# Optimization experiments

Hardware: AMD Instinct MI355X
Metric: run time of the kernel (lower is better)

## Reference

```python
import jax, jax.numpy as jnp
import numpy as np

N_QUBITS = 14
N_LAYERS = 2
LATENT_DIM = 14
DIM = 2 ** N_QUBITS
PAIRS = [(i, i + 1) for i in range(N_QUBITS - 1)]  # 'linear' entanglement


def _cnot_perm(control, target, n):
    # permutation of basis indices implementing CNOT(control, target)
    idx = np.arange(2 ** n)
    cbit = (idx >> (n - control - 1)) & 1
    flipped = np.where(cbit == 1, idx ^ (1 << (n - target - 1)), idx)
    return jnp.asarray(flipped)

CNOT_PERMS = [_cnot_perm(c, t, N_QUBITS) for c, t in PAIRS]


def _apply_1q(state, gate, q):
    # state: (B, 2^n) complex; gate: (2,2) or (B,2,2) complex
    B = state.shape[0]
    s = state.reshape(B, 2 ** (N_QUBITS - q - 1), 2, 2 ** q)
    if gate.ndim == 2:
        s = jnp.einsum('ij,bkjl->bkil', gate, s)
    else:
        s = jnp.einsum('bij,bkjl->bkil', gate, s)
    return s.reshape(B, DIM)


def _ry_batched(theta):
    c = jnp.cos(theta / 2)
    s = jnp.sin(theta / 2)
    g = jnp.stack([jnp.stack([c, -s], -1), jnp.stack([s, c], -1)], -2)  # (B,2,2)
    return g.astype(jnp.complex64)


def _ry(theta):
    c = jnp.cos(theta / 2)
    s = jnp.sin(theta / 2)
    return jnp.stack([jnp.stack([c, -s]), jnp.stack([s, c])]).astype(jnp.complex64)


def _rz(theta):
    th = theta.astype(jnp.complex64)
    e0 = jnp.exp(-0.5j * th)
    e1 = jnp.exp(0.5j * th)
    zero = jnp.zeros((), jnp.complex64)
    return jnp.stack([jnp.stack([e0, zero]), jnp.stack([zero, e1])])


def setup_inputs() -> dict:
    key = jax.random.key(0)
    k1, k2 = jax.random.split(key)
    latent = jax.random.normal(k1, (256, LATENT_DIM), dtype=jnp.float32)
    weights = jax.random.normal(k2, (N_LAYERS * N_QUBITS * 3,), dtype=jnp.float32) * 0.1
    return {"latent": latent, "weights": weights}


def reference(latent, weights):
    B = latent.shape[0]
    state = jnp.zeros((B, DIM), dtype=jnp.complex64).at[:, 0].set(1.0)
    # latent encoding: RY(pi * z_i) on qubit i
    for i in range(min(LATENT_DIM, N_QUBITS)):
        state = _apply_1q(state, _ry_batched(latent[:, i] * np.pi), i)
    # variational layers
    for layer in range(N_LAYERS):
        off = layer * N_QUBITS * 3
        for q in range(N_QUBITS):
            b = off + q * 3
            state = _apply_1q(state, _ry(weights[b]), q)
            state = _apply_1q(state, _rz(weights[b + 1]), q)
            state = _apply_1q(state, _ry(weights[b + 2]), q)
        for perm in CNOT_PERMS:
            state = state[:, perm]
    return jnp.abs(state) ** 2
```

## Files before the change

kernel.cpp:

```cpp
#include <hip/hip_runtime.h>


typedef float f32x2 __attribute__((ext_vector_type(2)));
typedef float f32x4 __attribute__((ext_vector_type(4)));

constexpr int NQ    = 14;
constexpr int DIM   = 1 << NQ;
constexpr int NT    = 512;
constexpr int SPLIT = 2;

__device__ __forceinline__ f32x2 cmul(f32x2 a, f32x2 b) {
    return f32x2{a.x * b.x - a.y * b.y, a.x * b.y + a.y * b.x};
}
__device__ __forceinline__ int g7(int x)  { return x ^ (x >> 1); }
__device__ __forceinline__ int g7i(int x) { x ^= x >> 1; x ^= x >> 2; x ^= x >> 4; return x; }

__global__ __launch_bounds__(NT)
void qsim_kernel(const float* __restrict__ latent,
                 const float* __restrict__ weights,
                 float* __restrict__ out)
{
    __shared__ f32x2 vq [2 * NQ];
    __shared__ f32x2 m1 [4 * NQ];
    __shared__ f32x2 plo[128], phi[128];
    __shared__ f32x2 cc0[128], cc1[128], dd0[128], dd1[128];
    __shared__ __align__(16) float fjx[128], fjy[128], fjz[128], fjw[128];
    __shared__ f32x4 eA[128];

    const int b   = blockIdx.x >> 1;
    const int qtr = blockIdx.x & 1;
    const int tid = threadIdx.x;

    if (tid < NQ) {
        const int q = tid;
        const float a = weights[3 * q] + 3.14159265358979323846f * latent[b * NQ + q];
        const float t = weights[3 * q + 1];
        const float c = weights[3 * q + 2];
        float ct, stt, cp, sp, cm, sm;
        __sincosf(0.5f * t, &stt, &ct);
        __sincosf(0.5f * (a + c), &sp, &cp);
        __sincosf(0.5f * (a - c), &sm, &cm);
        vq[2 * q + 0] = f32x2{ct * cp, -stt * cm};
        vq[2 * q + 1] = f32x2{ct * sp,  stt * sm};
    } else if (tid >= 64 && tid < 64 + NQ) {
        const int q = tid - 64;
        const float a = weights[3 * NQ + 3 * q];
        const float t = weights[3 * NQ + 3 * q + 1];
        const float c = weights[3 * NQ + 3 * q + 2];
        float ct, stt, cp, sp, cm, sm;
        __sincosf(0.5f * t, &stt, &ct);
        __sincosf(0.5f * (a + c), &sp, &cp);
        __sincosf(0.5f * (a - c), &sm, &cm);
        m1[4 * q + 0] = f32x2{ ct * cp, -stt * cm};
        m1[4 * q + 1] = f32x2{-ct * sp,  stt * sm};
        m1[4 * q + 2] = f32x2{ ct * sp,  stt * sm};
        m1[4 * q + 3] = f32x2{ ct * cp,  stt * cm};
    }
    __syncthreads();

    if (tid < 256) {
        const int half = tid >> 7;
        const int m    = tid & 127;
        const int qb   = half * 7;
        f32x2 p = {1.0f, 0.0f};
        #pragma unroll
        for (int j = 0; j < 7; ++j)
            p = cmul(p, vq[2 * (qb + j) + ((m >> j) & 1)]);
        (half ? phi : plo)[m] = p;
    }
    __syncthreads();

    if (tid < 256) {
        const int w    = tid >> 6;
        const int lane = tid & 63;
        const int u0 = 2 * lane, u1 = 2 * lane + 1;

        f32x2 r0, r1;
        if (w == 0)      { r0 = plo[g7(u0)];       r1 = plo[g7(u1)];       }
        else if (w == 1) { r0 = plo[g7(u0) ^ 64];  r1 = plo[g7(u1) ^ 64];  }
        else if (w == 2) { r0 = phi[g7(u0)];       r1 = f32x2{0.f, 0.f};   }
        else             { r0 = f32x2{0.f, 0.f};   r1 = phi[g7(u1)];       }

        const int mbase = (w >> 1) * 7;

        {
            const f32x2 M00 = m1[4 * mbase + 0], M01 = m1[4 * mbase + 1];
            const f32x2 M10 = m1[4 * mbase + 2], M11 = m1[4 * mbase + 3];
            const f32x2 n0 = cmul(M00, r0) + cmul(M01, r1);
            const f32x2 n1 = cmul(M10, r0) + cmul(M11, r1);
            r0 = n0; r1 = n1;
        }
        #pragma unroll
        for (int k = 1; k < 7; ++k) {
            const int q = mbase + k;
            const f32x2 M00 = m1[4 * q + 0], M01 = m1[4 * q + 1];
            const f32x2 M10 = m1[4 * q + 2], M11 = m1[4 * q + 3];
            const int msk = 1 << (k - 1);
            const int bit = (lane >> (k - 1)) & 1;
            f32x2 p0, p1;
            p0.x = __shfl_xor(r0.x, msk, 64); p0.y = __shfl_xor(r0.y, msk, 64);
            p1.x = __shfl_xor(r1.x, msk, 64); p1.y = __shfl_xor(r1.y, msk, 64);
            const f32x2 lo0 = bit ? p0 : r0, hi0 = bit ? r0 : p0;
            const f32x2 lo1 = bit ? p1 : r1, hi1 = bit ? r1 : p1;
            const f32x2 Ma  = bit ? M10 : M00;
            const f32x2 Mb  = bit ? M11 : M01;
            r0 = cmul(Ma, lo0) + cmul(Mb, hi0);
            r1 = cmul(Ma, lo1) + cmul(Mb, hi1);
        }
        const int j0 = g7i(u0), j1 = g7i(u1);
        if (w == 0)      { cc0[j0] = r0; cc0[j1] = r1; }
        else if (w == 1) { cc1[j0] = r0; cc1[j1] = r1; }
        else if (w == 2) { dd0[j0] = r0; dd0[j1] = r1; }
        else             { dd1[j0] = r0; dd1[j1] = r1; }
    }
    __syncthreads();

    if (tid < 128) {
        const int j = tid;
        const f32x2 c0 = cc0[j], c1 = cc1[j];
        fjx[j] = c0.x * c0.x + c0.y * c0.y;
        fjy[j] = c1.x * c1.x + c1.y * c1.y;
        fjz[j] = c0.x * c1.x + c0.y * c1.y;
        fjw[j] = c0.y * c1.x - c0.x * c1.y;
    } else if (tid < 256) {
        const int A = tid - 128;
        const f32x2 d0 = dd0[A], d1 = dd1[A];
        eA[A] = f32x4{d0.x * d0.x + d0.y * d0.y,
                      d1.x * d1.x + d1.y * d1.y,
                      2.0f * (d0.x * d1.x + d0.y * d1.y),
                     -2.0f * (d0.y * d1.x - d0.x * d1.y)};
    }
    __syncthreads();

    {
        const int w    = tid >> 6;
        const int lane = tid & 63;
        const int h    = lane >> 5;
        const int s    = lane & 31;

        const f32x4 fx = *(const f32x4*)&fjx[4 * s];
        const f32x4 fy = *(const f32x4*)&fjy[4 * s];
        const f32x4 fz = *(const f32x4*)&fjz[4 * s];
        const f32x4 fw = *(const f32x4*)&fjw[4 * s];

        const int row0 = qtr * 64 + 8 * w + h;
        const int col  = h ? (124 - 4 * s) : (4 * s);
        float* op = out + (size_t)b * DIM + row0 * 128 + col;

        #pragma unroll
        for (int t = 0; t < 4; ++t) {
            const f32x4 e = eA[row0 + 2 * t];
            f32x4 o = e.x * fx + e.y * fy + e.z * fz + e.w * fw;
            if (h) o = f32x4{o.w, o.z, o.y, o.x};
            *(f32x4*)(op + t * 256) = o;
        }
    }
}

extern "C" void kernel_launch(void* const* d_in, const int* in_sizes, int n_in,
                              void* d_out, int out_size, void* d_ws, size_t ws_size,
                              hipStream_t stream) {
    const float* latent  = (const float*)d_in[0];
    const float* weights = (const float*)d_in[1];
    float* out = (float*)d_out;

    const int B = in_sizes[0] / NQ;
    qsim_kernel<<<B * SPLIT, NT, 0, stream>>>(latent, weights, out);
}
```

Baseline: 11.56 us.

## Split simulation into table-build and output-expansion kernels via workspace

```diff
diff --git a/kernel.cpp b/kernel.cpp
--- a/kernel.cpp
+++ b/kernel.cpp
@@ -4,10 +4,8 @@
 typedef float f32x2 __attribute__((ext_vector_type(2)));
 typedef float f32x4 __attribute__((ext_vector_type(4)));
 
-constexpr int NQ    = 14;
-constexpr int DIM   = 1 << NQ;
-constexpr int NT    = 512;
-constexpr int SPLIT = 2;
+constexpr int NQ  = 14;
+constexpr int DIM = 1 << NQ;
 
 __device__ __forceinline__ f32x2 cmul(f32x2 a, f32x2 b) {
     return f32x2{a.x * b.x - a.y * b.y, a.x * b.y + a.y * b.x};
@@ -15,20 +13,17 @@
 __device__ __forceinline__ int g7(int x)  { return x ^ (x >> 1); }
 __device__ __forceinline__ int g7i(int x) { x ^= x >> 1; x ^= x >> 2; x ^= x >> 4; return x; }
 
-__global__ __launch_bounds__(NT)
-void qsim_kernel(const float* __restrict__ latent,
+__global__ __launch_bounds__(256)
+void qtab_kernel(const float* __restrict__ latent,
                  const float* __restrict__ weights,
-                 float* __restrict__ out)
+                 float* __restrict__ ws)
 {
     __shared__ f32x2 vq [2 * NQ];
     __shared__ f32x2 m1 [4 * NQ];
     __shared__ f32x2 plo[128], phi[128];
     __shared__ f32x2 cc0[128], cc1[128], dd0[128], dd1[128];
-    __shared__ __align__(16) float fjx[128], fjy[128], fjz[128], fjw[128];
-    __shared__ f32x4 eA[128];
 
-    const int b   = blockIdx.x >> 1;
-    const int qtr = blockIdx.x & 1;
+    const int b   = blockIdx.x;
     const int tid = threadIdx.x;
 
     if (tid < NQ) {
@@ -58,7 +53,7 @@
     }
     __syncthreads();
 
-    if (tid < 256) {
+    {
         const int half = tid >> 7;
         const int m    = tid & 127;
         const int qb   = half * 7;
@@ -70,7 +65,7 @@
     }
     __syncthreads();
 
-    if (tid < 256) {
+    {
         const int w    = tid >> 6;
         const int lane = tid & 63;
         const int u0 = 2 * lane, u1 = 2 * lane + 1;
@@ -115,46 +110,65 @@
     }
     __syncthreads();
 
+    float* tb = ws + (size_t)b * 1024;
     if (tid < 128) {
         const int j = tid;
         const f32x2 c0 = cc0[j], c1 = cc1[j];
-        fjx[j] = c0.x * c0.x + c0.y * c0.y;
-        fjy[j] = c1.x * c1.x + c1.y * c1.y;
-        fjz[j] = c0.x * c1.x + c0.y * c1.y;
-        fjw[j] = c0.y * c1.x - c0.x * c1.y;
-    } else if (tid < 256) {
+        tb[j +   0] = c0.x * c0.x + c0.y * c0.y;
+        tb[j + 128] = c1.x * c1.x + c1.y * c1.y;
+        tb[j + 256] = c0.x * c1.x + c0.y * c1.y;
+        tb[j + 384] = c0.y * c1.x - c0.x * c1.y;
+    } else {
         const int A = tid - 128;
         const f32x2 d0 = dd0[A], d1 = dd1[A];
-        eA[A] = f32x4{d0.x * d0.x + d0.y * d0.y,
-                      d1.x * d1.x + d1.y * d1.y,
-                      2.0f * (d0.x * d1.x + d0.y * d1.y),
-                     -2.0f * (d0.y * d1.x - d0.x * d1.y)};
+        ((f32x4*)(tb + 512))[A] =
+            f32x4{d0.x * d0.x + d0.y * d0.y,
+                  d1.x * d1.x + d1.y * d1.y,
+                  2.0f * (d0.x * d1.x + d0.y * d1.y),
+                 -2.0f * (d0.y * d1.x - d0.x * d1.y)};
     }
-    __syncthreads();
+}
 
-    {
-        const int w    = tid >> 6;
-        const int lane = tid & 63;
-        const int h    = lane >> 5;
-        const int s    = lane & 31;
+__global__ __launch_bounds__(256)
+void qout_kernel(const float* __restrict__ ws, float* __restrict__ out)
+{
+    const int b    = blockIdx.x >> 2;
+    const int qtr  = blockIdx.x & 3;
+    const int tid  = threadIdx.x;
+    const int w    = tid >> 6;
+    const int lane = tid & 63;
+    const int h    = lane >> 5;
+    const int s    = lane & 31;
 
-        const f32x4 fx = *(const f32x4*)&fjx[4 * s];
-        const f32x4 fy = *(const f32x4*)&fjy[4 * s];
-        const f32x4 fz = *(const f32x4*)&fjz[4 * s];
-        const f32x4 fw = *(const f32x4*)&fjw[4 * s];
+    const float* tb = ws + (size_t)b * 1024;
+    const f32x4 fx = *(const f32x4*)(tb +   0 + 4 * s);
+    const f32x4 fy = *(const f32x4*)(tb + 128 + 4 * s);
+    const f32x4 fz = *(const f32x4*)(tb + 256 + 4 * s);
+    const f32x4 fw = *(const f32x4*)(tb + 384 + 4 * s);
+    const f32x4* eA = (const f32x4*)(tb + 512);
 
-        const int row0 = qtr * 64 + 8 * w + h;
-        const int col  = h ? (124 - 4 * s) : (4 * s);
-        float* op = out + (size_t)b * DIM + row0 * 128 + col;
+    const int row0 = 32 * qtr + 8 * w + h;
+    const f32x4 e0 = eA[row0 + 0];
+    const f32x4 e1 = eA[row0 + 2];
+    const f32x4 e2 = eA[row0 + 4];
+    const f32x4 e3 = eA[row0 + 6];
 
-        #pragma unroll
-        for (int t = 0; t < 4; ++t) {
-            const f32x4 e = eA[row0 + 2 * t];
-            f32x4 o = e.x * fx + e.y * fy + e.z * fz + e.w * fw;
-            if (h) o = f32x4{o.w, o.z, o.y, o.x};
-            *(f32x4*)(op + t * 256) = o;
-        }
-    }
+    const int col = h ? (124 - 4 * s) : (4 * s);
+    float* op = out + (size_t)b * DIM + row0 * 128 + col;
+
+    f32x4 o;
+    o = e0.x * fx + e0.y * fy + e0.z * fz + e0.w * fw;
+    if (h) o = f32x4{o.w, o.z, o.y, o.x};
+    *(f32x4*)(op + 0 * 256) = o;
+    o = e1.x * fx + e1.y * fy + e1.z * fz + e1.w * fw;
+    if (h) o = f32x4{o.w, o.z, o.y, o.x};
+    *(f32x4*)(op + 1 * 256) = o;
+    o = e2.x * fx + e2.y * fy + e2.z * fz + e2.w * fw;
+    if (h) o = f32x4{o.w, o.z, o.y, o.x};
+    *(f32x4*)(op + 2 * 256) = o;
+    o = e3.x * fx + e3.y * fy + e3.z * fz + e3.w * fw;
+    if (h) o = f32x4{o.w, o.z, o.y, o.x};
+    *(f32x4*)(op + 3 * 256) = o;
 }
 
 extern "C" void kernel_launch(void* const* d_in, const int* in_sizes, int n_in,
@@ -163,7 +177,9 @@
     const float* latent  = (const float*)d_in[0];
     const float* weights = (const float*)d_in[1];
     float* out = (float*)d_out;
+    float* ws  = (float*)d_ws;
 
     const int B = in_sizes[0] / NQ;
-    qsim_kernel<<<B * SPLIT, NT, 0, stream>>>(latent, weights, out);
+    qtab_kernel<<<B,     256, 0, stream>>>(latent, weights, ws);
+    qout_kernel<<<B * 4, 256, 0, stream>>>(ws, out);
 }
```

Measured after the change: 14.91 us. 28.9% more time.

## Fuse product-state and bilinear stages, one 1024-thread block per sample

Applied to the files above, without the earlier changes.

```diff
diff --git a/kernel.cpp b/kernel.cpp
--- a/kernel.cpp
+++ b/kernel.cpp
@@ -4,10 +4,9 @@
 typedef float f32x2 __attribute__((ext_vector_type(2)));
 typedef float f32x4 __attribute__((ext_vector_type(4)));
 
-constexpr int NQ    = 14;
-constexpr int DIM   = 1 << NQ;
-constexpr int NT    = 512;
-constexpr int SPLIT = 2;
+constexpr int NQ  = 14;
+constexpr int DIM = 1 << NQ;
+constexpr int NT  = 1024;
 
 __device__ __forceinline__ f32x2 cmul(f32x2 a, f32x2 b) {
     return f32x2{a.x * b.x - a.y * b.y, a.x * b.y + a.y * b.x};
@@ -22,13 +21,9 @@
 {
     __shared__ f32x2 vq [2 * NQ];
     __shared__ f32x2 m1 [4 * NQ];
-    __shared__ f32x2 plo[128], phi[128];
     __shared__ f32x2 cc0[128], cc1[128], dd0[128], dd1[128];
-    __shared__ __align__(16) float fjx[128], fjy[128], fjz[128], fjw[128];
-    __shared__ f32x4 eA[128];
 
-    const int b   = blockIdx.x >> 1;
-    const int qtr = blockIdx.x & 1;
+    const int b   = blockIdx.x;
     const int tid = threadIdx.x;
 
     if (tid < NQ) {
@@ -59,27 +54,31 @@
     __syncthreads();
 
     if (tid < 256) {
-        const int half = tid >> 7;
-        const int m    = tid & 127;
-        const int qb   = half * 7;
-        f32x2 p = {1.0f, 0.0f};
-        #pragma unroll
-        for (int j = 0; j < 7; ++j)
-            p = cmul(p, vq[2 * (qb + j) + ((m >> j) & 1)]);
-        (half ? phi : plo)[m] = p;
-    }
-    __syncthreads();
-
-    if (tid < 256) {
         const int w    = tid >> 6;
         const int lane = tid & 63;
-        const int u0 = 2 * lane, u1 = 2 * lane + 1;
+        const int u0   = 2 * lane;
+        const int m0   = g7(u0);
+        const int base = (w >> 1) * 14;
 
+        f32x2 t = vq[base + 2 + ((m0 >> 1) & 1)];
+        #pragma unroll
+        for (int j = 2; j < 6; ++j)
+            t = cmul(t, vq[base + 2 * j + ((m0 >> j) & 1)]);
+        const int b6 = ((m0 >> 6) & 1) ^ (w == 1 ? 1 : 0);
+        t = cmul(t, vq[base + 12 + b6]);
+
+        const int bit0 = m0 & 1;
         f32x2 r0, r1;
-        if (w == 0)      { r0 = plo[g7(u0)];       r1 = plo[g7(u1)];       }
-        else if (w == 1) { r0 = plo[g7(u0) ^ 64];  r1 = plo[g7(u1) ^ 64];  }
-        else if (w == 2) { r0 = phi[g7(u0)];       r1 = f32x2{0.f, 0.f};   }
-        else             { r0 = f32x2{0.f, 0.f};   r1 = phi[g7(u1)];       }
+        if (w < 2) {
+            r0 = cmul(t, vq[base + bit0]);
+            r1 = cmul(t, vq[base + (bit0 ^ 1)]);
+        } else if (w == 2) {
+            r0 = cmul(t, vq[base + bit0]);
+            r1 = f32x2{0.f, 0.f};
+        } else {
+            r0 = f32x2{0.f, 0.f};
+            r1 = cmul(t, vq[base + (bit0 ^ 1)]);
+        }
 
         const int mbase = (w >> 1) * 7;
 
@@ -107,28 +106,11 @@
             r0 = cmul(Ma, lo0) + cmul(Mb, hi0);
             r1 = cmul(Ma, lo1) + cmul(Mb, hi1);
         }
-        const int j0 = g7i(u0), j1 = g7i(u1);
+        const int j0 = g7i(u0), j1 = g7i(u0 + 1);
         if (w == 0)      { cc0[j0] = r0; cc0[j1] = r1; }
         else if (w == 1) { cc1[j0] = r0; cc1[j1] = r1; }
         else if (w == 2) { dd0[j0] = r0; dd0[j1] = r1; }
         else             { dd1[j0] = r0; dd1[j1] = r1; }
-    }
-    __syncthreads();
-
-    if (tid < 128) {
-        const int j = tid;
-        const f32x2 c0 = cc0[j], c1 = cc1[j];
-        fjx[j] = c0.x * c0.x + c0.y * c0.y;
-        fjy[j] = c1.x * c1.x + c1.y * c1.y;
-        fjz[j] = c0.x * c1.x + c0.y * c1.y;
-        fjw[j] = c0.y * c1.x - c0.x * c1.y;
-    } else if (tid < 256) {
-        const int A = tid - 128;
-        const f32x2 d0 = dd0[A], d1 = dd1[A];
-        eA[A] = f32x4{d0.x * d0.x + d0.y * d0.y,
-                      d1.x * d1.x + d1.y * d1.y,
-                      2.0f * (d0.x * d1.x + d0.y * d1.y),
-                     -2.0f * (d0.y * d1.x - d0.x * d1.y)};
     }
     __syncthreads();
 
@@ -138,19 +120,33 @@
         const int h    = lane >> 5;
         const int s    = lane & 31;
 
-        const f32x4 fx = *(const f32x4*)&fjx[4 * s];
-        const f32x4 fy = *(const f32x4*)&fjy[4 * s];
-        const f32x4 fz = *(const f32x4*)&fjz[4 * s];
-        const f32x4 fw = *(const f32x4*)&fjw[4 * s];
+        const f32x4* c0v = (const f32x4*)cc0;
+        const f32x4* c1v = (const f32x4*)cc1;
+        const f32x4 c0a = c0v[2 * s], c0b = c0v[2 * s + 1];
+        const f32x4 c1a = c1v[2 * s], c1b = c1v[2 * s + 1];
 
-        const int row0 = qtr * 64 + 8 * w + h;
+        const f32x4 fx = {c0a.x * c0a.x + c0a.y * c0a.y, c0a.z * c0a.z + c0a.w * c0a.w,
+                          c0b.x * c0b.x + c0b.y * c0b.y, c0b.z * c0b.z + c0b.w * c0b.w};
+        const f32x4 fy = {c1a.x * c1a.x + c1a.y * c1a.y, c1a.z * c1a.z + c1a.w * c1a.w,
+                          c1b.x * c1b.x + c1b.y * c1b.y, c1b.z * c1b.z + c1b.w * c1b.w};
+        const f32x4 fz = {c0a.x * c1a.x + c0a.y * c1a.y, c0a.z * c1a.z + c0a.w * c1a.w,
+                          c0b.x * c1b.x + c0b.y * c1b.y, c0b.z * c1b.z + c0b.w * c1b.w};
+        const f32x4 fw = {c0a.y * c1a.x - c0a.x * c1a.y, c0a.w * c1a.z - c0a.z * c1a.w,
+                          c0b.y * c1b.x - c0b.x * c1b.y, c0b.w * c1b.z - c0b.z * c1b.w};
+
+        const int row0 = 8 * w + h;
         const int col  = h ? (124 - 4 * s) : (4 * s);
         float* op = out + (size_t)b * DIM + row0 * 128 + col;
 
         #pragma unroll
         for (int t = 0; t < 4; ++t) {
-            const f32x4 e = eA[row0 + 2 * t];
-            f32x4 o = e.x * fx + e.y * fy + e.z * fz + e.w * fw;
+            const int A = row0 + 2 * t;
+            const f32x2 d0 = dd0[A], d1 = dd1[A];
+            const float ex = d0.x * d0.x + d0.y * d0.y;
+            const float ey = d1.x * d1.x + d1.y * d1.y;
+            const float ez =  2.0f * (d0.x * d1.x + d0.y * d1.y);
+            const float ew = -2.0f * (d0.y * d1.x - d0.x * d1.y);
+            f32x4 o = ex * fx + ey * fy + ez * fz + ew * fw;
             if (h) o = f32x4{o.w, o.z, o.y, o.x};
             *(f32x4*)(op + t * 256) = o;
         }
@@ -165,5 +161,5 @@
     float* out = (float*)d_out;
 
     const int B = in_sizes[0] / NQ;
-    qsim_kernel<<<B * SPLIT, NT, 0, stream>>>(latent, weights, out);
+    qsim_kernel<<<B, NT, 0, stream>>>(latent, weights, out);
 }
```

New measurement: 11.39 us. No clear change (-1.5%).
